# Kernel tuning notes

Measured on AMD Instinct MI355X. Metric: run time of the kernel, lower is better.

Reference implementation:

```python
import jax, jax.numpy as jnp
import numpy as np

DIM = 2048
N_HEADS = 16
N_KV = 4
HEAD_DIM = DIM // N_HEADS  # 128
B, S = 2, 2048
EPS = float(np.finfo(np.float32).eps)  # torch RMSNorm eps=None -> finfo eps


def _rotate_half(x):
    # interleaved-pair rotation: out[..., ::2] = -x[..., 1::2]; out[..., 1::2] = x[..., ::2]
    x2 = x.reshape(x.shape[:-1] + (HEAD_DIM // 2, 2))
    rot = jnp.stack([-x2[..., 1], x2[..., 0]], axis=-1)
    return rot.reshape(x.shape)


def _rmsnorm(x, w):
    var = jnp.mean(x * x, axis=-1, keepdims=True)
    return x * jax.lax.rsqrt(var + EPS) * w


def setup_inputs() -> dict:
    key = jax.random.key(0)
    ks = jax.random.split(key, 5)
    out_f = (N_HEADS + 2 * N_KV) * HEAD_DIM  # 3072
    return {
        "x": jax.random.normal(ks[0], (B, S, DIM), jnp.float32),
        "wqkv": jax.random.normal(ks[1], (out_f, DIM), jnp.float32) * (2.0 / (DIM + out_f)) ** 0.5,
        "wo": jax.random.normal(ks[2], (DIM, DIM), jnp.float32) * (1.0 / DIM) ** 0.5,
        "q_norm_w": jnp.ones((HEAD_DIM,), jnp.float32),
        "k_norm_w": jnp.ones((HEAD_DIM,), jnp.float32),
        "freqs_cos": jnp.cos(jax.random.normal(ks[3], (S, 1, HEAD_DIM), jnp.float32)),
        "freqs_sin": jnp.sin(jax.random.normal(ks[4], (S, 1, HEAD_DIM), jnp.float32)),
    }


def reference(x, wqkv, wo, q_norm_w, k_norm_w, freqs_cos, freqs_sin):
    b, s, _ = x.shape
    qkv = jnp.einsum("bsd,od->bso", x, wqkv)
    q_size = N_HEADS * HEAD_DIM
    kv_size = N_KV * HEAD_DIM
    xq = qkv[..., :q_size].reshape(b, s, N_HEADS, HEAD_DIM)
    xk = qkv[..., q_size:q_size + kv_size].reshape(b, s, N_KV, HEAD_DIM)
    xv = qkv[..., q_size + kv_size:].reshape(b, s, N_KV, HEAD_DIM)
    xq = _rmsnorm(xq, q_norm_w)
    xk = _rmsnorm(xk, k_norm_w)
    # RoPE (freqs broadcast over batch and heads)
    xq = xq * freqs_cos + _rotate_half(xq) * freqs_sin
    xk = xk * freqs_cos + _rotate_half(xk) * freqs_sin
    # GQA: group query heads per kv head instead of materializing repeats
    rep = N_HEADS // N_KV
    q = xq.transpose(0, 2, 1, 3).reshape(b, N_KV, rep, s, HEAD_DIM)
    k = xk.transpose(0, 2, 1, 3)  # [b, kv, s, d]
    v = xv.transpose(0, 2, 1, 3)
    scale = 1.0 / jnp.sqrt(jnp.asarray(HEAD_DIM, x.dtype))
    scores = jnp.einsum("bhgqd,bhkd->bhgqk", q, k) * scale
    probs = jax.nn.softmax(scores, axis=-1)
    attn = jnp.einsum("bhgqk,bhkd->bhgqd", probs, v)
    attn = attn.reshape(b, N_HEADS, s, HEAD_DIM).transpose(0, 2, 1, 3).reshape(b, s, DIM)
    return jnp.einsum("bsd,od->bso", attn, wo)
```

## Files before the change

kernel.cpp:

```cpp
#include <hip/hip_runtime.h>
#include <hip/hip_bf16.h>

typedef unsigned short u16;
typedef __bf16 bf16x8 __attribute__((ext_vector_type(8)));
typedef __bf16 bf16x4 __attribute__((ext_vector_type(4)));
typedef u16 u16x8 __attribute__((ext_vector_type(8)));
typedef float f32x4 __attribute__((ext_vector_type(4)));
typedef float f32x16 __attribute__((ext_vector_type(16)));

__device__ __forceinline__ u16 f2bf(float f) {
    unsigned u = __float_as_uint(f);
    return (u16)((u + 0x7fffu + ((u >> 16) & 1u)) >> 16);
}
__device__ __forceinline__ unsigned pkbf2(float a, float b) {
    __hip_bfloat162 h = __float22bfloat162_rn(make_float2(a, b));
    return *(unsigned*)&h;
}

__device__ __forceinline__ void gload16(const u16* g, u16* l) {
    __builtin_amdgcn_global_load_lds(
        (const __attribute__((address_space(1))) void*)g,
        (__attribute__((address_space(3))) void*)l, 16, 0, 0);
}

__device__ __forceinline__ void block_sync() {
    __builtin_amdgcn_sched_barrier(0);
    __builtin_amdgcn_s_barrier();
    __builtin_amdgcn_sched_barrier(0);
}
template<int N> __device__ __forceinline__ void waitvm() {
    if constexpr (N == 0)      asm volatile("s_waitcnt vmcnt(0)" ::: "memory");
    else if constexpr (N == 3) asm volatile("s_waitcnt vmcnt(3)" ::: "memory");
    else if constexpr (N == 4) asm volatile("s_waitcnt vmcnt(4)" ::: "memory");
    else if constexpr (N == 6) asm volatile("s_waitcnt vmcnt(6)" ::: "memory");
    else                       asm volatile("s_waitcnt vmcnt(8)" ::: "memory");
}

#define CVT_N1 2097152
#define CVT_N2 3670016
#define CVT_TOT 4718592
__global__ void cvt_all(const float* __restrict__ x, const float* __restrict__ wqkv,
                        const float* __restrict__ wo, u16* __restrict__ xb,
                        u16* __restrict__ wqkvb, u16* __restrict__ wob) {
    for (int i = blockIdx.x * 256 + threadIdx.x; i < CVT_TOT; i += 4608 * 256) {
        const float* s; u16* d; int j;
        if (i < CVT_N1)      { s = x;    d = xb;    j = i; }
        else if (i < CVT_N2) { s = wqkv; d = wqkvb; j = i - CVT_N1; }
        else                 { s = wo;   d = wob;   j = i - CVT_N2; }
        float4 v = *(const float4*)(s + (size_t)j * 4);
        uint2 o; o.x = pkbf2(v.x, v.y); o.y = pkbf2(v.z, v.w);
        *(uint2*)(d + (size_t)j * 4) = o;
    }
}

template<int ROWS>
__device__ __forceinline__ void stage32(const u16* __restrict__ g, int K,
                                        int k0, u16* l, int tid) {
#pragma unroll
    for (int s = 0; s < ROWS / 128; ++s) {
        int row = s * 128 + (tid >> 2);
        int sc = (tid & 3) ^ ((tid >> 2) & 3);
        gload16(g + (size_t)row * K + k0 + sc * 8, l + s * 4096 + tid * 8);
    }
}

template<int BM, int BN>
__device__ __forceinline__ void gemm_pipeline(const u16* __restrict__ Ab,
                                              const u16* __restrict__ Bb, int K,
                                              u16* sAll,
                                              f32x4 (&acc)[BM / 32][BN / 64],
                                              int tid) {
    constexpr int MR = BM / 32, NR = BN / 64;
    constexpr int TILE = (BM + BN) * 32;
    constexpr int NLD = (BM + BN) / 128;
    const int lane = tid & 63, wave = tid >> 6;
    const int quad = lane >> 4, l16 = lane & 15;
    const int wm = wave >> 2, wn = wave & 3;
    const int ar0 = wm * (BM / 2) + l16;
    const int br0 = wn * (BN / 4) + l16;

    stage32<BM>(Ab, K, 0, sAll, tid);
    stage32<BN>(Bb, K, 0, sAll + BM * 32, tid);
    stage32<BM>(Ab, K, 32, sAll + TILE, tid);
    stage32<BN>(Bb, K, 32, sAll + TILE + BM * 32, tid);

    const int nt = K >> 5;
    int bufc = 0, bufn = 2;
    for (int t = 0; t < nt; ++t) {
        if (t < nt - 1) waitvm<NLD>();
        else            waitvm<0>();
        block_sync();
        if (t + 2 < nt) {
            u16* nb = sAll + bufn * TILE;
            stage32<BM>(Ab, K, (t + 2) * 32, nb, tid);
            stage32<BN>(Bb, K, (t + 2) * 32, nb + BM * 32, tid);
        }
        const u16* cA = sAll + bufc * TILE;
        const u16* cB = cA + BM * 32;
        bf16x8 af[MR], bf[NR];
#pragma unroll
        for (int m = 0; m < MR; ++m) {
            int r = ar0 + m * 16;
            af[m] = *(const bf16x8*)&cA[r * 32 + ((quad ^ (r & 3)) * 8)];
        }
#pragma unroll
        for (int n = 0; n < NR; ++n) {
            int r = br0 + n * 16;
            bf[n] = *(const bf16x8*)&cB[r * 32 + ((quad ^ (r & 3)) * 8)];
        }
        __builtin_amdgcn_s_setprio(1);
#pragma unroll
        for (int m = 0; m < MR; ++m)
#pragma unroll
            for (int n = 0; n < NR; ++n)
                acc[m][n] = __builtin_amdgcn_mfma_f32_16x16x32_bf16(
                    af[m], bf[n], acc[m][n], 0, 0, 0);
        __builtin_amdgcn_s_setprio(0);
        bufc = (bufc == 2) ? 0 : bufc + 1;
        bufn = (bufn == 2) ? 0 : bufn + 1;
    }
}

__global__ __launch_bounds__(512, 2)
void gemm_bt(const u16* __restrict__ A, const u16* __restrict__ B,
             float* __restrict__ C, int M, int N, int K) {
    __shared__ u16 sAll[3 * (128 + 256) * 32];
    const int tid = threadIdx.x;
    const int wave = tid >> 6, lane = tid & 63;
    const int quad = lane >> 4, l16 = lane & 15;
    const int wm = wave >> 2, wn = wave & 3;
    const int bid = blockIdx.x;
    const int xcd = bid & 7, r2 = bid >> 3;
    const int bni = (xcd & 1) * 4 + (r2 & 3);
    const int bmi = (xcd >> 1) * 8 + (r2 >> 2);
    const size_t bm = (size_t)bmi * 128, bn = (size_t)bni * 256;
    f32x4 acc[4][4] = {};
    gemm_pipeline<128, 256>(A + bm * K, B + bn * K, K, sAll, acc, tid);
#pragma unroll
    for (int m = 0; m < 4; ++m)
#pragma unroll
        for (int n = 0; n < 4; ++n)
#pragma unroll
            for (int r = 0; r < 4; ++r)
                C[(bm + wm * 64 + m * 16 + quad * 4 + r) * (size_t)N +
                  bn + wn * 64 + n * 16 + l16] = acc[m][n][r];
}

__global__ __launch_bounds__(512, 2)
void gemm_qkv(const u16* __restrict__ xb, const u16* __restrict__ wq,
              const float* __restrict__ qw, const float* __restrict__ kw,
              const float* __restrict__ fcos, const float* __restrict__ fsin,
              u16* __restrict__ qb, u16* __restrict__ kb, u16* __restrict__ vt) {
    __shared__ u16 sAll[3 * (256 + 256) * 32];
    const int tid = threadIdx.x;
    const int wave = tid >> 6, lane = tid & 63;
    const int quad = lane >> 4, l16 = lane & 15;
    const int wm = wave >> 2, wn = wave & 3;
    const int bid = blockIdx.x;
    const int xcd = bid & 7, r2 = bid >> 3;
    const int bx = (xcd & 1) * 6 + r2 % 6;
    const int by = (xcd >> 1) * 4 + r2 / 6;
    f32x4 acc[8][4] = {};
    gemm_pipeline<256, 256>(xb + (size_t)by * 256 * 2048,
                            wq + (size_t)bx * 256 * 2048, 2048, sAll, acc, tid);

    const int b = by >> 3;
    const int sb = (by & 7) * 256 + wm * 128;
    const int headh = wn >> 1;
    const int dcol0 = (wn & 1) * 64;

    if (bx >= 10) {
        const int qp = ((quad & 1) << 1) | (quad >> 1);
        const int kvh = (bx - 10) * 2 + headh;
        u16* base = vt + (size_t)(b * 4 + kvh) * 128 * 2048;
#pragma unroll
        for (int m = 0; m < 8; ++m) {
            int s0 = sb + m * 16 + qp * 4;
#pragma unroll
            for (int n = 0; n < 4; ++n) {
                int d = dcol0 + n * 16 + l16;
                bf16x4 pv;
#pragma unroll
                for (int r = 0; r < 4; ++r) pv[r] = (__bf16)acc[m][n][r];
                *(bf16x4*)(base + (size_t)d * 2048 + s0) = pv;
            }
        }
        return;
    }

    float* red = (float*)sAll;
    float ssq[8][4];
#pragma unroll
    for (int m = 0; m < 8; ++m)
#pragma unroll
        for (int r = 0; r < 4; ++r) {
            float t = 0.f;
#pragma unroll
            for (int n = 0; n < 4; ++n) t += acc[m][n][r] * acc[m][n][r];
#pragma unroll
            for (int off = 1; off <= 8; off <<= 1) t += __shfl_xor(t, off);
            ssq[m][r] = t;
        }
    __syncthreads();
    if (l16 == 0)
#pragma unroll
        for (int m = 0; m < 8; ++m)
#pragma unroll
            for (int r = 0; r < 4; ++r)
                red[((wn & 1) * 2 + headh) * 256 + wm * 128 + m * 16 + quad * 4 + r] =
                    ssq[m][r];
    __syncthreads();

    const bool isQ = bx < 8;
    const float qscl = isQ ? 0.08838834764831845f * 1.4426950408889634f : 1.0f;
    const float* wp = isQ ? qw : kw;
    float wcol[4];
#pragma unroll
    for (int n = 0; n < 4; ++n) wcol[n] = wp[dcol0 + n * 16 + l16];
    u16* dstbase = isQ ? qb + (size_t)(b * 16 + bx * 2 + headh) * 2048 * 128
                       : kb + (size_t)(b * 4 + (bx - 8) * 2 + headh) * 2048 * 128;
    const float sgn = (l16 & 1) ? 1.f : -1.f;

#pragma unroll
    for (int m = 0; m < 8; ++m) {
#pragma unroll
        for (int r = 0; r < 4; ++r) {
            int rowl = wm * 128 + m * 16 + quad * 4 + r;
            float var = (red[(0 + headh) * 256 + rowl] +
                         red[(2 + headh) * 256 + rowl]) * (1.0f / 128.0f);
            float rms = rsqrtf(var + 1.1920928955078125e-07f) * qscl;
            int s = sb + m * 16 + quad * 4 + r;
            const float* fc = fcos + (size_t)s * 128 + dcol0;
            const float* fn = fsin + (size_t)s * 128 + dcol0;
            u16* drow = dstbase + (size_t)s * 128 + dcol0;
#pragma unroll
            for (int n = 0; n < 4; ++n) {
                float y = acc[m][n][r] * rms * wcol[n];
                float yp = __shfl_xor(y, 1);
                float o = y * fc[n * 16 + l16] + sgn * yp * fn[n * 16 + l16];
                drow[n * 16 + l16] = f2bf(o);
            }
        }
    }
}

#define KBUF(c) ((c) * 8192)
#define VBUF 16384
__global__ __launch_bounds__(256, 3)
void flash_attn(const u16* __restrict__ qb, const u16* __restrict__ kb,
                const u16* __restrict__ vt, u16* __restrict__ ab) {
    __shared__ u16 smem[24576];
    __shared__ float Llds[128];

    const int tid = threadIdx.x;
    const int wave = tid >> 6, lane = tid & 63;
    const int hf = lane >> 5, c32 = lane & 31;
    const int bid = blockIdx.x;
    const int swz = (bid & 7) * 64 + (bid >> 3);
    const int qt = swz & 15, bh = swz >> 4;
    const int hh = bh & 15, bb = bh >> 4;
    const int kh = hh >> 2;

    const u16* Qbase = qb + (size_t)(bb * 16 + hh) * 2048 * 128;
    const u16* Kbase = kb + (size_t)(bb * 4 + kh) * 2048 * 128;
    const u16* Vbase = vt + (size_t)(bb * 4 + kh) * 128 * 2048;

    bf16x8 aq[8];
#pragma unroll
    for (int kq = 0; kq < 8; ++kq)
        aq[kq] = *(const bf16x8*)(Qbase +
            (size_t)(qt * 128 + wave * 32 + c32) * 128 + kq * 16 + hf * 8);

    f32x16 O[4] = {};
    float lacc = 0.f;

    const int krow = tid >> 4;
    const u16* kg = Kbase + (size_t)krow * 128 + (((tid & 15) ^ (krow & 7)) * 8);
    const int vrow = tid >> 3;
    const u16* vg = Vbase + (size_t)vrow * 2048 + (((tid & 7) ^ (vrow & 7)) * 8);

    auto stageK = [&](int buf, int key0) {
#pragma unroll
        for (int s = 0; s < 4; ++s)
            gload16(kg + key0 * 128 + s * 2048, &smem[KBUF(buf) + s * 2048 + tid * 8]);
    };
    auto stageV = [&](int key0) {
#pragma unroll
        for (int s = 0; s < 4; ++s)
            gload16(vg + (size_t)s * 65536 + key0, &smem[VBUF + s * 2048 + tid * 8]);
    };

    stageK(0, 0);
    stageV(0);

    for (int kt = 0; kt < 32; ++kt) {
        const int cur = kt & 1;
        if (kt < 31) {
            stageK(cur ^ 1, (kt + 1) * 64);
            waitvm<8>();
        } else {
            waitvm<0>();
        }
        block_sync();

        f32x16 sc[2] = {};
        __builtin_amdgcn_s_setprio(1);
#pragma unroll
        for (int kq = 0; kq < 8; ++kq) {
#pragma unroll
            for (int mt = 0; mt < 2; ++mt) {
                bf16x8 kf = *(const bf16x8*)&smem[KBUF(cur) + (mt * 32 + c32) * 128 +
                                                 (((kq * 2 + hf) ^ (c32 & 7)) * 8)];
                sc[mt] = __builtin_amdgcn_mfma_f32_32x32x16_bf16(kf, aq[kq], sc[mt], 0, 0, 0);
            }
        }
        __builtin_amdgcn_s_setprio(0);

        int pdw[2][8];
#pragma unroll
        for (int mt = 0; mt < 2; ++mt) {
            float p[16];
#pragma unroll
            for (int r = 0; r < 16; ++r) p[r] = __builtin_amdgcn_exp2f(sc[mt][r]);
            float a0 = (p[0] + p[1]) + (p[2] + p[3]);
            float a1 = (p[4] + p[5]) + (p[6] + p[7]);
            float a2 = (p[8] + p[9]) + (p[10] + p[11]);
            float a3 = (p[12] + p[13]) + (p[14] + p[15]);
            lacc += (a0 + a1) + (a2 + a3);
#pragma unroll
            for (int i = 0; i < 8; ++i) pdw[mt][i] = (int)pkbf2(p[2 * i], p[2 * i + 1]);
        }

        if (kt < 31) waitvm<4>();
        else         waitvm<0>();
        block_sync();

        __builtin_amdgcn_s_setprio(1);
#pragma unroll
        for (int kc = 0; kc < 4; ++kc) {
            const int mt = kc >> 1, L = kc & 1;
            union { int i[4]; bf16x8 v; } u;
            u.i[0] = pdw[mt][4 * L + 0];
            u.i[1] = pdw[mt][4 * L + 1];
            u.i[2] = pdw[mt][4 * L + 2];
            u.i[3] = pdw[mt][4 * L + 3];
#pragma unroll
            for (int dt = 0; dt < 4; ++dt) {
                bf16x8 vf = *(const bf16x8*)&smem[VBUF + (dt * 32 + c32) * 64 +
                                                 (((kc * 2 + hf) ^ (c32 & 7)) * 8)];
                O[dt] = __builtin_amdgcn_mfma_f32_32x32x16_bf16(u.v, vf, O[dt], 0, 0, 0);
            }
        }
        __builtin_amdgcn_s_setprio(0);
        block_sync();
        if (kt < 31) stageV((kt + 1) * 64);
    }

    float l = lacc + __shfl_xor(lacc, 32);
    if (hf == 0) Llds[wave * 32 + c32] = l;

    float inv[16];
#pragma unroll
    for (int r = 0; r < 16; ++r)
        inv[r] = __builtin_amdgcn_rcpf(Llds[wave * 32 + (r & 3) + 8 * (r >> 2) + 4 * hf]);

    u16* scr = &smem[wave * 32 * 136];
#pragma unroll
    for (int dt = 0; dt < 4; ++dt)
#pragma unroll
        for (int r = 0; r < 16; ++r) {
            int q_r = (r & 3) + 8 * (r >> 2) + 4 * hf;
            scr[q_r * 136 + dt * 32 + c32] = f2bf(O[dt][r] * inv[r]);
        }
#pragma unroll
    for (int it = 0; it < 8; ++it) {
        int f = it * 64 + lane;
        int row = f >> 4, c = f & 15;
        u16x8 v = *(const u16x8*)&scr[row * 136 + c * 8];
        int qg = qt * 128 + wave * 32 + row;
        *(u16x8*)(ab + ((size_t)(bb * 2048 + qg)) * 2048 + hh * 128 + c * 8) = v;
    }
}

extern "C" void kernel_launch(void* const* d_in, const int* in_sizes, int n_in,
                              void* d_out, int out_size, void* d_ws, size_t ws_size,
                              hipStream_t stream) {
    const float* x    = (const float*)d_in[0];
    const float* wqkv = (const float*)d_in[1];
    const float* wo   = (const float*)d_in[2];
    const float* qw   = (const float*)d_in[3];
    const float* kw   = (const float*)d_in[4];
    const float* fc   = (const float*)d_in[5];
    const float* fs   = (const float*)d_in[6];
    float* out = (float*)d_out;
    char* ws = (char*)d_ws;

    u16* xb    = (u16*)(ws + 0);
    u16* wqkvb = (u16*)(ws + 16777216);
    u16* wob   = (u16*)(ws + 29360128);
    u16* qb    = (u16*)(ws + 37748736);
    u16* kb    = (u16*)(ws + 54525952);
    u16* vt    = (u16*)(ws + 58720256);
    u16* ab    = (u16*)(ws + 62914560);

    cvt_all<<<4608, 256, 0, stream>>>(x, wqkv, wo, xb, wqkvb, wob);
    gemm_qkv<<<192, 512, 0, stream>>>(xb, wqkvb, qw, kw, fc, fs, qb, kb, vt);
    flash_attn<<<512, 256, 0, stream>>>(qb, kb, vt, ab);
    gemm_bt<<<256, 512, 0, stream>>>(ab, wob, out, 4096, 2048, 2048);
}
```

Baseline: 297.7 us.

## Replace QKV GEMM pipeline with double-buffered K=64 tiles and phased MFMA scheduling

The QKV projection GEMM stops using the shared triple-buffered K=32 pipeline and gets its own loop. It stages 64-wide K tiles into two LDS buffers with an XOR swizzle. Each K step is split into four quadrant phases that load A/B fragments from LDS, issue the next tile's global-to-LDS loads, and run MFMAs at raised priority between barriers. The aim is to halve the number of K iterations and to overlap LDS reads and global prefetch with matrix math. In exchange it adds many more barriers per iteration and a larger LDS footprint (128 KB), which may affect the intended two-blocks-per-CU occupancy.

```diff
diff --git a/kernel.cpp b/kernel.cpp
--- a/kernel.cpp
+++ b/kernel.cpp
@@ -26,6 +26,10 @@
 __device__ __forceinline__ void block_sync() {
     __builtin_amdgcn_sched_barrier(0);
     __builtin_amdgcn_s_barrier();
+    __builtin_amdgcn_sched_barrier(0);
+}
+__device__ __forceinline__ void waitlgkm() {
+    asm volatile("s_waitcnt lgkmcnt(0)" ::: "memory");
     __builtin_amdgcn_sched_barrier(0);
 }
 template<int N> __device__ __forceinline__ void waitvm() {
@@ -53,6 +57,16 @@
     }
 }
 
+template<int ROWS>
+__device__ __forceinline__ void stage64(const u16* __restrict__ g, int K,
+                                        int k0, u16* l, int tid) {
+#pragma unroll
+    for (int s = 0; s < ROWS / 64; ++s) {
+        int row = s * 64 + (tid >> 3);
+        int sc = (tid & 7) ^ ((tid >> 3) & 7);
+        gload16(g + (size_t)row * K + k0 + sc * 8, l + s * 4096 + tid * 8);
+    }
+}
 template<int ROWS>
 __device__ __forceinline__ void stage32(const u16* __restrict__ g, int K,
                                         int k0, u16* l, int tid) {
@@ -151,7 +165,7 @@
               const float* __restrict__ qw, const float* __restrict__ kw,
               const float* __restrict__ fcos, const float* __restrict__ fsin,
               u16* __restrict__ qb, u16* __restrict__ kb, u16* __restrict__ vt) {
-    __shared__ u16 sAll[3 * (256 + 256) * 32];
+    __shared__ u16 sAll[2 * (256 + 256) * 64];
     const int tid = threadIdx.x;
     const int wave = tid >> 6, lane = tid & 63;
     const int quad = lane >> 4, l16 = lane & 15;
@@ -160,9 +174,77 @@
     const int xcd = bid & 7, r2 = bid >> 3;
     const int bx = (xcd & 1) * 6 + r2 % 6;
     const int by = (xcd >> 1) * 4 + r2 / 6;
+
+    const u16* Ab = xb + (size_t)by * 256 * 2048;
+    const u16* Bb = wq + (size_t)bx * 256 * 2048;
+    constexpr int K = 2048, TILE = 512 * 64;
+
+    const int ar0 = wm * 128 + l16;
+    const int br0 = wn * 64 + l16;
     f32x4 acc[8][4] = {};
-    gemm_pipeline<256, 256>(xb + (size_t)by * 256 * 2048,
-                            wq + (size_t)bx * 256 * 2048, 2048, sAll, acc, tid);
+    bf16x8 af[4][2], bf[2][2];
+
+    stage64<256>(Ab, K, 0, sAll, tid);
+    stage64<256>(Bb, K, 0, sAll + 256 * 64, tid);
+    waitvm<0>();
+    block_sync();
+
+    const int nt = K / 64;
+    for (int t = 0; t < nt; ++t) {
+        const int cur = t & 1, nxt = cur ^ 1;
+        const u16* cA = sAll + cur * TILE;
+        const u16* cB = cA + 256 * 64;
+        u16* nA = sAll + nxt * TILE;
+        u16* nB = nA + 256 * 64;
+
+        auto LDA = [&](int mh) {
+#pragma unroll
+            for (int mm = 0; mm < 4; ++mm) {
+                int r = ar0 + (mh * 4 + mm) * 16;
+#pragma unroll
+                for (int kk = 0; kk < 2; ++kk)
+                    af[mm][kk] = *(const bf16x8*)&cA[r * 64 +
+                        (((kk * 4 + quad) ^ (r & 7)) * 8)];
+            }
+        };
+        auto LDB = [&](int nh) {
+#pragma unroll
+            for (int nn = 0; nn < 2; ++nn) {
+                int r = br0 + (nh * 2 + nn) * 16;
+#pragma unroll
+                for (int kk = 0; kk < 2; ++kk)
+                    bf[nn][kk] = *(const bf16x8*)&cB[r * 64 +
+                        (((kk * 4 + quad) ^ (r & 7)) * 8)];
+            }
+        };
+        auto MM = [&](int mh, int nh) {
+            __builtin_amdgcn_s_setprio(1);
+#pragma unroll
+            for (int mm = 0; mm < 4; ++mm)
+#pragma unroll
+                for (int nn = 0; nn < 2; ++nn)
+#pragma unroll
+                    for (int kk = 0; kk < 2; ++kk)
+                        acc[mh * 4 + mm][nh * 2 + nn] =
+                            __builtin_amdgcn_mfma_f32_16x16x32_bf16(
+                                af[mm][kk], bf[nn][kk],
+                                acc[mh * 4 + mm][nh * 2 + nn], 0, 0, 0);
+            __builtin_amdgcn_s_setprio(0);
+        };
+
+        LDA(0); LDB(0);
+        if (t + 1 < nt) stage64<256>(Ab, K, (t + 1) * 64, nA, tid);
+        block_sync(); waitlgkm(); MM(0, 0); block_sync();
+        LDB(1);
+        if (t + 1 < nt) stage64<256>(Bb, K, (t + 1) * 64, nB, tid);
+        block_sync(); waitlgkm(); MM(0, 1); block_sync();
+        LDA(1);
+        block_sync(); waitlgkm(); MM(1, 1); block_sync();
+        LDB(0);
+        block_sync(); waitlgkm(); MM(1, 0);
+        waitvm<0>();
+        block_sync();
+    }
 
     const int b = by >> 3;
     const int sb = (by & 7) * 256 + wm * 128;
```

Result: no change. 300.2 us (+0.8%).
